# Kernel tuning notes

Measured on AMD Instinct MI355X. Metric: run time of the kernel, lower is better.

Reference implementation:

```python
import jax, jax.numpy as jnp
import numpy as np

N_NODES = 100000
N_EDGES = 1600000
D_IN = 128
D_OUT = 128


def setup_inputs() -> dict:
    key = jax.random.key(0)
    k1, k2, k3, k4, k5, k6 = jax.random.split(key, 6)
    x = jax.random.normal(k1, (N_NODES, D_IN), dtype=jnp.float32)
    edge_row = jax.random.randint(k2, (N_EDGES,), 0, N_NODES, dtype=jnp.int64)
    edge_col = jax.random.randint(k3, (N_EDGES,), 0, N_NODES, dtype=jnp.int64)
    edge_val = jax.random.uniform(k4, (N_EDGES,), dtype=jnp.float32)
    # Xavier-uniform init for weight, zeros for bias (matches reset_parameters)
    limit = float(np.sqrt(6.0 / (D_IN + D_OUT)))
    weight = jax.random.uniform(k5, (D_IN, D_OUT), minval=-limit, maxval=limit, dtype=jnp.float32)
    bias = jax.random.normal(k6, (D_OUT,), dtype=jnp.float32) * 0.02
    return {"x": x, "edge_row": edge_row, "edge_col": edge_col,
            "edge_val": edge_val, "weight": weight, "bias": bias}


def reference(x, edge_row, edge_col, edge_val, weight, bias):
    # dropout(p=0.0) is identity in eval -> omitted
    support = x @ weight                       # [N, D_OUT] dense GEMM
    # SpMM: out[r] = sum_{e: row[e]==r} val[e] * support[col[e]]
    messages = edge_val[:, None] * support[edge_col]   # [E, D_OUT]
    out = jax.ops.segment_sum(messages, edge_row, num_segments=N_NODES)
    return out + bias
```

## Files before the change

kernel.cpp:

```cpp
#include <hip/hip_runtime.h>


#define DMODEL 128
#define CAP 56
#define BROWS 256
#define BCAP 5120
#define NB_SC 800
#define SC_CHUNK 2000
#define SC_EPT 8
#define MAXBUCK 400

typedef __attribute__((ext_vector_type(8))) short short8_t;
typedef __attribute__((ext_vector_type(4))) float float4_t;

__device__ inline short f2bf(float f) {
    unsigned u = __float_as_uint(f);
    return (short)((u + 0x7FFFu + ((u >> 16) & 1u)) >> 16);
}

__global__ __launch_bounds__(256) void prep_kernel(const float* __restrict__ w,
                                                   unsigned short* __restrict__ wsw,
                                                   int* __restrict__ cursor, int nbuck) {
    if (blockIdx.x < 8) {
        int c = blockIdx.x * 256 + threadIdx.x;
        int lane = c & 63;
        int kcnt = c >> 6;
        int kc = kcnt & 3, nt = kcnt >> 2;
        int n  = nt * 16 + (lane & 15);
        int k0 = kc * 32 + (lane >> 4) * 8;
        short8_t v;
        #pragma unroll
        for (int j = 0; j < 8; ++j)
            v[j] = f2bf(w[(size_t)(k0 + j) * DMODEL + n]);
        *(short8_t*)&wsw[(size_t)c * 8] = v;
    } else {
        for (int j = threadIdx.x; j < nbuck; j += 256) cursor[j] = 0;
    }
}

__global__ __launch_bounds__(256) void scatter_kernel(
    const int* __restrict__ erow, const int* __restrict__ ecol,
    const float* __restrict__ eval,
    int* __restrict__ cursor, uint2* __restrict__ rec, int n_edges, int nbuck)
{
    __shared__ int cnt[MAXBUCK];
    __shared__ int gb[MAXBUCK];
    for (int j = threadIdx.x; j < nbuck; j += 256) cnt[j] = 0;
    __syncthreads();

    int base = blockIdx.x * SC_CHUNK;
    int lr[SC_EPT];
    #pragma unroll
    for (int i = 0; i < SC_EPT; ++i) {
        int e = base + threadIdx.x + i * 256;
        lr[i] = -1;
        if (threadIdx.x + i * 256 < SC_CHUNK && e < n_edges) {
            int b = erow[e] >> 8;
            lr[i] = atomicAdd(&cnt[b], 1);
        }
    }
    __syncthreads();
    for (int j = threadIdx.x; j < nbuck; j += 256) {
        int c = cnt[j];
        gb[j] = c ? atomicAdd(&cursor[j], c) : 0;
    }
    __syncthreads();
    #pragma unroll
    for (int i = 0; i < SC_EPT; ++i) {
        if (lr[i] >= 0) {
            int e = base + threadIdx.x + i * 256;
            int r = erow[e];
            int b = r >> 8;
            int pos = gb[b] + lr[i];
            if (pos < BCAP) {
                unsigned q = (unsigned)(eval[e] * 32767.0f + 0.5f);
                uint2 v;
                v.x = (q << 17) | (unsigned)ecol[e];
                v.y = (unsigned)(r & (BROWS - 1));
                rec[(size_t)b * BCAP + pos] = v;
            }
        }
    }
}

__global__ __launch_bounds__(256) void bucket_insert_kernel(
    const int* __restrict__ cursor, const uint2* __restrict__ rec,
    int* __restrict__ counts, unsigned* __restrict__ edata, int n_nodes)
{
    int b = blockIdx.x;
    __shared__ int cnt2[BROWS];
    cnt2[threadIdx.x] = 0;
    __syncthreads();

    int cb = cursor[b]; if (cb > BCAP) cb = BCAP;
    const uint2* rb = rec + (size_t)b * BCAP;
    for (int j = threadIdx.x; j < cb; j += 256) {
        uint2 v = rb[j];
        int rl = (int)v.y;
        int rk = atomicAdd(&cnt2[rl], 1);
        if (rk < CAP) {
            int row = (b << 8) + rl;
            edata[(size_t)row * CAP + rk] = v.x;
        }
    }
    __syncthreads();
    int row = (b << 8) + (int)threadIdx.x;
    if (row < n_nodes) counts[row] = cnt2[threadIdx.x];
}

__global__ __launch_bounds__(256) void gemm_kernel(
    const float* __restrict__ x, const unsigned short* __restrict__ wsw,
    unsigned short* __restrict__ support, int n_nodes)
{
    int wv   = threadIdx.x >> 6;
    int lane = threadIdx.x & 63;
    int m    = lane & 15;
    int g    = lane >> 4;

    int rowA  = blockIdx.x * 64 + wv * 16 + m;
    int rowAc = rowA < n_nodes ? rowA : n_nodes - 1;
    const float* xr = x + (size_t)rowAc * DMODEL + g * 8;

    short8_t af[4];
    #pragma unroll
    for (int kc = 0; kc < 4; ++kc) {
        float4 u0 = *(const float4*)(xr + kc * 32);
        float4 u1 = *(const float4*)(xr + kc * 32 + 4);
        short8_t a;
        a[0] = f2bf(u0.x); a[1] = f2bf(u0.y); a[2] = f2bf(u0.z); a[3] = f2bf(u0.w);
        a[4] = f2bf(u1.x); a[5] = f2bf(u1.y); a[6] = f2bf(u1.z); a[7] = f2bf(u1.w);
        af[kc] = a;
    }

    const short8_t* wf = (const short8_t*)wsw;

    float4_t acc[8];
    #pragma unroll
    for (int nt = 0; nt < 8; ++nt) {
        float4_t z = {0.f, 0.f, 0.f, 0.f};
        acc[nt] = z;
        #pragma unroll
        for (int kc = 0; kc < 4; ++kc) {
            short8_t bf = wf[(nt * 4 + kc) * 64 + lane];
            acc[nt] = __builtin_amdgcn_mfma_f32_16x16x32_bf16(af[kc], bf, acc[nt], 0, 0, 0);
        }
    }

    int orow = blockIdx.x * 64 + wv * 16 + g * 4;
    #pragma unroll
    for (int r = 0; r < 4; ++r) {
        int row = orow + r;
        if (row < n_nodes) {
            #pragma unroll
            for (int nt = 0; nt < 8; ++nt)
                support[(size_t)row * DMODEL + nt * 16 + m] = (unsigned short)f2bf(acc[nt][r]);
        }
    }
}

__global__ __launch_bounds__(256) void aggregate_kernel(
    const int* __restrict__ counts, const unsigned* __restrict__ edata,
    const uint4* __restrict__ sup, const float* __restrict__ bias,
    float* __restrict__ out, int n_nodes)
{
    int node = (blockIdx.x * blockDim.x + threadIdx.x) >> 6;
    if (node >= n_nodes) return;
    int lane = threadIdx.x & 63;
    int sub  = lane >> 4;
    int q    = lane & 15;

    int len = counts[node];
    if (len > CAP) len = CAP;
    const unsigned* ed = edata + (size_t)node * CAP;

    float acc[8];
    #pragma unroll
    for (int k = 0; k < 8; ++k) acc[k] = 0.f;

    const float SCL = 1.0f / 32767.0f;

    #define EDGE_FMA(rec, p)                                                 \
        {                                                                    \
            float v = (float)((rec) >> 17) * SCL;                            \
            acc[0] = fmaf(v, __uint_as_float((p).x << 16), acc[0]);          \
            acc[1] = fmaf(v, __uint_as_float((p).x & 0xFFFF0000u), acc[1]);  \
            acc[2] = fmaf(v, __uint_as_float((p).y << 16), acc[2]);          \
            acc[3] = fmaf(v, __uint_as_float((p).y & 0xFFFF0000u), acc[3]);  \
            acc[4] = fmaf(v, __uint_as_float((p).z << 16), acc[4]);          \
            acc[5] = fmaf(v, __uint_as_float((p).z & 0xFFFF0000u), acc[5]);  \
            acc[6] = fmaf(v, __uint_as_float((p).w << 16), acc[6]);          \
            acc[7] = fmaf(v, __uint_as_float((p).w & 0xFFFF0000u), acc[7]);  \
        }

    int i = sub;
    for (; i + 12 < len; i += 16) {
        unsigned r0 = ed[i];
        unsigned r1 = ed[i + 4];
        unsigned r2 = ed[i + 8];
        unsigned r3 = ed[i + 12];
        uint4 p0 = sup[(size_t)(r0 & 0x1FFFFu) * 16 + q];
        uint4 p1 = sup[(size_t)(r1 & 0x1FFFFu) * 16 + q];
        uint4 p2 = sup[(size_t)(r2 & 0x1FFFFu) * 16 + q];
        uint4 p3 = sup[(size_t)(r3 & 0x1FFFFu) * 16 + q];
        EDGE_FMA(r0, p0);
        EDGE_FMA(r1, p1);
        EDGE_FMA(r2, p2);
        EDGE_FMA(r3, p3);
    }
    for (; i < len; i += 4) {
        unsigned r0 = ed[i];
        uint4 p0 = sup[(size_t)(r0 & 0x1FFFFu) * 16 + q];
        EDGE_FMA(r0, p0);
    }
    #undef EDGE_FMA

    #pragma unroll
    for (int k = 0; k < 8; ++k) {
        acc[k] += __shfl_xor(acc[k], 16);
        acc[k] += __shfl_xor(acc[k], 32);
    }

    if (sub == 0) {
        float4 b0 = ((const float4*)bias)[q * 2];
        float4 b1 = ((const float4*)bias)[q * 2 + 1];
        float4_t o0 = {acc[0] + b0.x, acc[1] + b0.y, acc[2] + b0.z, acc[3] + b0.w};
        float4_t o1 = {acc[4] + b1.x, acc[5] + b1.y, acc[6] + b1.z, acc[7] + b1.w};
        __builtin_nontemporal_store(o0, (float4_t*)out + (size_t)node * 32 + q * 2);
        __builtin_nontemporal_store(o1, (float4_t*)out + (size_t)node * 32 + q * 2 + 1);
    }
}

extern "C" void kernel_launch(void* const* d_in, const int* in_sizes, int n_in,
                              void* d_out, int out_size, void* d_ws, size_t ws_size,
                              hipStream_t stream) {
    const float* x      = (const float*)d_in[0];
    const int*   erow   = (const int*)d_in[1];
    const int*   ecol   = (const int*)d_in[2];
    const float* eval   = (const float*)d_in[3];
    const float* weight = (const float*)d_in[4];
    const float* bias   = (const float*)d_in[5];
    float* out = (float*)d_out;

    const int n_nodes = in_sizes[0] / DMODEL;
    const int n_edges = in_sizes[3];
    const int nbuck   = (n_nodes + BROWS - 1) / BROWS;

    char* ws = (char*)d_ws;
    unsigned short* support = (unsigned short*)ws;
    uint2*          rec     = (uint2*)ws;
    ws += (size_t)n_nodes * DMODEL * 2;
    unsigned short* wsw     = (unsigned short*)ws;  ws += (size_t)DMODEL * DMODEL * 2;
    int*      counts = (int*)ws;                    ws += ((size_t)n_nodes * 4 + 15) & ~15ull;
    int*      cursor = (int*)ws;                    ws += ((size_t)nbuck * 4 + 15) & ~15ull;
    unsigned* edata  = (unsigned*)ws;               ws += (size_t)n_nodes * CAP * 4;

    const int nb_g = (n_nodes + 63) / 64;

    prep_kernel<<<9, 256, 0, stream>>>(weight, wsw, cursor, nbuck);
    scatter_kernel<<<NB_SC, 256, 0, stream>>>(erow, ecol, eval, cursor, rec, n_edges, nbuck);
    bucket_insert_kernel<<<nbuck, 256, 0, stream>>>(cursor, rec, counts, edata, n_nodes);
    gemm_kernel<<<nb_g, 256, 0, stream>>>(x, wsw, support, n_nodes);
    aggregate_kernel<<<(n_nodes + 3) / 4, 256, 0, stream>>>(
        counts, edata, (const uint4*)support, bias, out, n_nodes);
}
```

Measured before the change: 248.6 us.

## Slice support matrix by column blocks so aggregation gathers stay cache-resident

The GEMM now writes support in a column-sliced layout: 8 slices of 16 bf16 columns, each holding all nodes contiguously. Aggregation runs one block per (node chunk, slice), with 16 lanes per node, each lane pair covering a 32-byte row slice. Consecutive blocks cycle through slices, so each slice (about 3.2 MB) can stay hot in L2 during random gathers. The cost is that edge records are re-read once per slice, gathers shrink to 32-byte segments, and lane utilization drops for low-degree nodes.

```diff
diff --git a/kernel.cpp b/kernel.cpp
--- a/kernel.cpp
+++ b/kernel.cpp
@@ -9,6 +9,7 @@
 #define SC_CHUNK 2000
 #define SC_EPT 8
 #define MAXBUCK 400
+#define NSLICE 8
 
 typedef __attribute__((ext_vector_type(8))) short short8_t;
 typedef __attribute__((ext_vector_type(4))) float float4_t;
@@ -153,25 +154,29 @@
         if (row < n_nodes) {
             #pragma unroll
             for (int nt = 0; nt < 8; ++nt)
-                support[(size_t)row * DMODEL + nt * 16 + m] = (unsigned short)f2bf(acc[nt][r]);
+                support[((size_t)nt * n_nodes + row) * 16 + m] = (unsigned short)f2bf(acc[nt][r]);
         }
     }
 }
 
 __global__ __launch_bounds__(256) void aggregate_kernel(
     const int* __restrict__ counts, const unsigned* __restrict__ edata,
-    const uint4* __restrict__ sup, const float* __restrict__ bias,
+    const unsigned short* __restrict__ sup_s, const float* __restrict__ bias,
     float* __restrict__ out, int n_nodes)
 {
-    int node = (blockIdx.x * blockDim.x + threadIdx.x) >> 6;
+    int slice  = blockIdx.x & (NSLICE - 1);
+    int nchunk = blockIdx.x >> 3;
+    int grp  = threadIdx.x >> 4;
+    int node = nchunk * 16 + grp;
     if (node >= n_nodes) return;
-    int lane = threadIdx.x & 63;
-    int sub  = lane >> 4;
-    int q    = lane & 15;
+    int l    = threadIdx.x & 15;
+    int slot = l >> 1;
+    int half = l & 1;
 
     int len = counts[node];
     if (len > CAP) len = CAP;
     const unsigned* ed = edata + (size_t)node * CAP;
+    const unsigned short* sb = sup_s + (size_t)slice * n_nodes * 16;
 
     float acc[8];
     #pragma unroll
@@ -192,41 +197,38 @@
             acc[7] = fmaf(v, __uint_as_float((p).w & 0xFFFF0000u), acc[7]);  \
         }
 
-    int i = sub;
-    for (; i + 12 < len; i += 16) {
+    int i = slot;
+    for (; i + 8 < len; i += 16) {
         unsigned r0 = ed[i];
-        unsigned r1 = ed[i + 4];
-        unsigned r2 = ed[i + 8];
-        unsigned r3 = ed[i + 12];
-        uint4 p0 = sup[(size_t)(r0 & 0x1FFFFu) * 16 + q];
-        uint4 p1 = sup[(size_t)(r1 & 0x1FFFFu) * 16 + q];
-        uint4 p2 = sup[(size_t)(r2 & 0x1FFFFu) * 16 + q];
-        uint4 p3 = sup[(size_t)(r3 & 0x1FFFFu) * 16 + q];
+        unsigned r1 = ed[i + 8];
+        uint4 p0 = *(const uint4*)(sb + (size_t)(r0 & 0x1FFFFu) * 16 + half * 8);
+        uint4 p1 = *(const uint4*)(sb + (size_t)(r1 & 0x1FFFFu) * 16 + half * 8);
         EDGE_FMA(r0, p0);
         EDGE_FMA(r1, p1);
-        EDGE_FMA(r2, p2);
-        EDGE_FMA(r3, p3);
-    }
-    for (; i < len; i += 4) {
+    }
+    for (; i < len; i += 8) {
         unsigned r0 = ed[i];
-        uint4 p0 = sup[(size_t)(r0 & 0x1FFFFu) * 16 + q];
+        uint4 p0 = *(const uint4*)(sb + (size_t)(r0 & 0x1FFFFu) * 16 + half * 8);
         EDGE_FMA(r0, p0);
     }
     #undef EDGE_FMA
 
     #pragma unroll
     for (int k = 0; k < 8; ++k) {
-        acc[k] += __shfl_xor(acc[k], 16);
-        acc[k] += __shfl_xor(acc[k], 32);
-    }
-
-    if (sub == 0) {
-        float4 b0 = ((const float4*)bias)[q * 2];
-        float4 b1 = ((const float4*)bias)[q * 2 + 1];
+        acc[k] += __shfl_xor(acc[k], 2);
+        acc[k] += __shfl_xor(acc[k], 4);
+        acc[k] += __shfl_xor(acc[k], 8);
+    }
+
+    if (slot == 0) {
+        int col0 = slice * 16 + half * 8;
+        float4 b0 = *(const float4*)(bias + col0);
+        float4 b1 = *(const float4*)(bias + col0 + 4);
         float4_t o0 = {acc[0] + b0.x, acc[1] + b0.y, acc[2] + b0.z, acc[3] + b0.w};
         float4_t o1 = {acc[4] + b1.x, acc[5] + b1.y, acc[6] + b1.z, acc[7] + b1.w};
-        __builtin_nontemporal_store(o0, (float4_t*)out + (size_t)node * 32 + q * 2);
-        __builtin_nontemporal_store(o1, (float4_t*)out + (size_t)node * 32 + q * 2 + 1);
+        float* op = out + (size_t)node * DMODEL + col0;
+        __builtin_nontemporal_store(o0, (float4_t*)op);
+        __builtin_nontemporal_store(o1, (float4_t*)(op + 4));
     }
 }
 
@@ -254,12 +256,13 @@
     int*      cursor = (int*)ws;                    ws += ((size_t)nbuck * 4 + 15) & ~15ull;
     unsigned* edata  = (unsigned*)ws;               ws += (size_t)n_nodes * CAP * 4;
 
-    const int nb_g = (n_nodes + 63) / 64;
+    const int nb_g  = (n_nodes + 63) / 64;
+    const int nb_ag = NSLICE * ((n_nodes + 15) / 16);
 
     prep_kernel<<<9, 256, 0, stream>>>(weight, wsw, cursor, nbuck);
     scatter_kernel<<<NB_SC, 256, 0, stream>>>(erow, ecol, eval, cursor, rec, n_edges, nbuck);
     bucket_insert_kernel<<<nbuck, 256, 0, stream>>>(cursor, rec, counts, edata, n_nodes);
     gemm_kernel<<<nb_g, 256, 0, stream>>>(x, wsw, support, n_nodes);
-    aggregate_kernel<<<(n_nodes + 3) / 4, 256, 0, stream>>>(
-        counts, edata, (const uint4*)support, bias, out, n_nodes);
-}
+    aggregate_kernel<<<nb_ag, 256, 0, stream>>>(
+        counts, edata, support, bias, out, n_nodes);
+}
```

Result: slower. 289.8 us (+16.6%).

## Fuse bucket grouping into aggregation via shared-memory per-row edge lists

Applied to the files above, without the earlier changes.

Removes the bucket_insert kernel and the global edata/counts arrays. Each aggregation block now loads its bucket's records, groups them by row in LDS, and then aggregates 32 rows per wave. Buckets are halved to 128 rows, and each cursor counter is padded to its own cache line to cut atomic contention. This saves a kernel launch and a global write/read of the grouped edges. The cost is about 28KB of LDS per block, which limits occupancy, and fewer blocks (782) each doing serial per-node loops with long-latency gathers.

```diff
diff --git a/kernel.cpp b/kernel.cpp
--- a/kernel.cpp
+++ b/kernel.cpp
@@ -3,12 +3,14 @@
 
 #define DMODEL 128
 #define CAP 56
-#define BROWS 256
-#define BCAP 5120
+#define BROWS 128
+#define BSHIFT 7
+#define BCAP 2560
 #define NB_SC 800
 #define SC_CHUNK 2000
 #define SC_EPT 8
-#define MAXBUCK 400
+#define MAXBUCK 800
+#define CURPAD 16
 
 typedef __attribute__((ext_vector_type(8))) short short8_t;
 typedef __attribute__((ext_vector_type(4))) float float4_t;
@@ -20,7 +22,7 @@
 
 __global__ __launch_bounds__(256) void prep_kernel(const float* __restrict__ w,
                                                    unsigned short* __restrict__ wsw,
-                                                   int* __restrict__ cursor, int nbuck) {
+                                                   int* __restrict__ cursor, int n_cursor) {
     if (blockIdx.x < 8) {
         int c = blockIdx.x * 256 + threadIdx.x;
         int lane = c & 63;
@@ -34,7 +36,7 @@
             v[j] = f2bf(w[(size_t)(k0 + j) * DMODEL + n]);
         *(short8_t*)&wsw[(size_t)c * 8] = v;
     } else {
-        for (int j = threadIdx.x; j < nbuck; j += 256) cursor[j] = 0;
+        for (int j = threadIdx.x; j < n_cursor; j += 256) cursor[j] = 0;
     }
 }
 
@@ -55,14 +57,14 @@
         int e = base + threadIdx.x + i * 256;
         lr[i] = -1;
         if (threadIdx.x + i * 256 < SC_CHUNK && e < n_edges) {
-            int b = erow[e] >> 8;
+            int b = erow[e] >> BSHIFT;
             lr[i] = atomicAdd(&cnt[b], 1);
         }
     }
     __syncthreads();
     for (int j = threadIdx.x; j < nbuck; j += 256) {
         int c = cnt[j];
-        gb[j] = c ? atomicAdd(&cursor[j], c) : 0;
+        gb[j] = c ? atomicAdd(&cursor[j * CURPAD], c) : 0;
     }
     __syncthreads();
     #pragma unroll
@@ -70,7 +72,7 @@
         if (lr[i] >= 0) {
             int e = base + threadIdx.x + i * 256;
             int r = erow[e];
-            int b = r >> 8;
+            int b = r >> BSHIFT;
             int pos = gb[b] + lr[i];
             if (pos < BCAP) {
                 unsigned q = (unsigned)(eval[e] * 32767.0f + 0.5f);
@@ -83,31 +85,6 @@
     }
 }
 
-__global__ __launch_bounds__(256) void bucket_insert_kernel(
-    const int* __restrict__ cursor, const uint2* __restrict__ rec,
-    int* __restrict__ counts, unsigned* __restrict__ edata, int n_nodes)
-{
-    int b = blockIdx.x;
-    __shared__ int cnt2[BROWS];
-    cnt2[threadIdx.x] = 0;
-    __syncthreads();
-
-    int cb = cursor[b]; if (cb > BCAP) cb = BCAP;
-    const uint2* rb = rec + (size_t)b * BCAP;
-    for (int j = threadIdx.x; j < cb; j += 256) {
-        uint2 v = rb[j];
-        int rl = (int)v.y;
-        int rk = atomicAdd(&cnt2[rl], 1);
-        if (rk < CAP) {
-            int row = (b << 8) + rl;
-            edata[(size_t)row * CAP + rk] = v.x;
-        }
-    }
-    __syncthreads();
-    int row = (b << 8) + (int)threadIdx.x;
-    if (row < n_nodes) counts[row] = cnt2[threadIdx.x];
-}
-
 __global__ __launch_bounds__(256) void gemm_kernel(
     const float* __restrict__ x, const unsigned short* __restrict__ wsw,
     unsigned short* __restrict__ support, int n_nodes)
@@ -158,75 +135,94 @@
     }
 }
 
-__global__ __launch_bounds__(256) void aggregate_kernel(
-    const int* __restrict__ counts, const unsigned* __restrict__ edata,
+__global__ __launch_bounds__(256) void bucket_aggregate_kernel(
+    const int* __restrict__ cursor, const uint2* __restrict__ rec,
     const uint4* __restrict__ sup, const float* __restrict__ bias,
     float* __restrict__ out, int n_nodes)
 {
-    int node = (blockIdx.x * blockDim.x + threadIdx.x) >> 6;
-    if (node >= n_nodes) return;
+    int b = blockIdx.x;
+    __shared__ unsigned grouped[BROWS * CAP];
+    __shared__ int cnt[BROWS];
+    for (int j = threadIdx.x; j < BROWS; j += 256) cnt[j] = 0;
+    __syncthreads();
+
+    int cb = cursor[b * CURPAD]; if (cb > BCAP) cb = BCAP;
+    const uint2* rb = rec + (size_t)b * BCAP;
+    for (int j = threadIdx.x; j < cb; j += 256) {
+        uint2 v = rb[j];
+        int rl = (int)v.y;
+        int rk = atomicAdd(&cnt[rl], 1);
+        if (rk < CAP) grouped[rl * CAP + rk] = v.x;
+    }
+    __syncthreads();
+
+    int wv   = threadIdx.x >> 6;
     int lane = threadIdx.x & 63;
     int sub  = lane >> 4;
     int q    = lane & 15;
 
-    int len = counts[node];
-    if (len > CAP) len = CAP;
-    const unsigned* ed = edata + (size_t)node * CAP;
-
-    float acc[8];
-    #pragma unroll
-    for (int k = 0; k < 8; ++k) acc[k] = 0.f;
-
     const float SCL = 1.0f / 32767.0f;
 
-    #define EDGE_FMA(rec, p)                                                 \
-        {                                                                    \
-            float v = (float)((rec) >> 17) * SCL;                            \
-            acc[0] = fmaf(v, __uint_as_float((p).x << 16), acc[0]);          \
-            acc[1] = fmaf(v, __uint_as_float((p).x & 0xFFFF0000u), acc[1]);  \
-            acc[2] = fmaf(v, __uint_as_float((p).y << 16), acc[2]);          \
-            acc[3] = fmaf(v, __uint_as_float((p).y & 0xFFFF0000u), acc[3]);  \
-            acc[4] = fmaf(v, __uint_as_float((p).z << 16), acc[4]);          \
-            acc[5] = fmaf(v, __uint_as_float((p).z & 0xFFFF0000u), acc[5]);  \
-            acc[6] = fmaf(v, __uint_as_float((p).w << 16), acc[6]);          \
-            acc[7] = fmaf(v, __uint_as_float((p).w & 0xFFFF0000u), acc[7]);  \
-        }
-
-    int i = sub;
-    for (; i + 12 < len; i += 16) {
-        unsigned r0 = ed[i];
-        unsigned r1 = ed[i + 4];
-        unsigned r2 = ed[i + 8];
-        unsigned r3 = ed[i + 12];
-        uint4 p0 = sup[(size_t)(r0 & 0x1FFFFu) * 16 + q];
-        uint4 p1 = sup[(size_t)(r1 & 0x1FFFFu) * 16 + q];
-        uint4 p2 = sup[(size_t)(r2 & 0x1FFFFu) * 16 + q];
-        uint4 p3 = sup[(size_t)(r3 & 0x1FFFFu) * 16 + q];
-        EDGE_FMA(r0, p0);
-        EDGE_FMA(r1, p1);
-        EDGE_FMA(r2, p2);
-        EDGE_FMA(r3, p3);
-    }
-    for (; i < len; i += 4) {
-        unsigned r0 = ed[i];
-        uint4 p0 = sup[(size_t)(r0 & 0x1FFFFu) * 16 + q];
-        EDGE_FMA(r0, p0);
-    }
-    #undef EDGE_FMA
-
-    #pragma unroll
-    for (int k = 0; k < 8; ++k) {
-        acc[k] += __shfl_xor(acc[k], 16);
-        acc[k] += __shfl_xor(acc[k], 32);
-    }
-
-    if (sub == 0) {
-        float4 b0 = ((const float4*)bias)[q * 2];
-        float4 b1 = ((const float4*)bias)[q * 2 + 1];
-        float4_t o0 = {acc[0] + b0.x, acc[1] + b0.y, acc[2] + b0.z, acc[3] + b0.w};
-        float4_t o1 = {acc[4] + b1.x, acc[5] + b1.y, acc[6] + b1.z, acc[7] + b1.w};
-        __builtin_nontemporal_store(o0, (float4_t*)out + (size_t)node * 32 + q * 2);
-        __builtin_nontemporal_store(o1, (float4_t*)out + (size_t)node * 32 + q * 2 + 1);
+    for (int nl = wv * 32; nl < wv * 32 + 32; ++nl) {
+        int node = (b << BSHIFT) + nl;
+        if (node >= n_nodes) break;
+        int len = cnt[nl];
+        if (len > CAP) len = CAP;
+        const unsigned* ed = &grouped[nl * CAP];
+
+        float acc[8];
+        #pragma unroll
+        for (int k = 0; k < 8; ++k) acc[k] = 0.f;
+
+        #define EDGE_FMA(rec_, p)                                                \
+            {                                                                    \
+                float v = (float)((rec_) >> 17) * SCL;                           \
+                acc[0] = fmaf(v, __uint_as_float((p).x << 16), acc[0]);          \
+                acc[1] = fmaf(v, __uint_as_float((p).x & 0xFFFF0000u), acc[1]);  \
+                acc[2] = fmaf(v, __uint_as_float((p).y << 16), acc[2]);          \
+                acc[3] = fmaf(v, __uint_as_float((p).y & 0xFFFF0000u), acc[3]);  \
+                acc[4] = fmaf(v, __uint_as_float((p).z << 16), acc[4]);          \
+                acc[5] = fmaf(v, __uint_as_float((p).z & 0xFFFF0000u), acc[5]);  \
+                acc[6] = fmaf(v, __uint_as_float((p).w << 16), acc[6]);          \
+                acc[7] = fmaf(v, __uint_as_float((p).w & 0xFFFF0000u), acc[7]);  \
+            }
+
+        int i = sub;
+        for (; i + 12 < len; i += 16) {
+            unsigned r0 = ed[i];
+            unsigned r1 = ed[i + 4];
+            unsigned r2 = ed[i + 8];
+            unsigned r3 = ed[i + 12];
+            uint4 p0 = sup[(size_t)(r0 & 0x1FFFFu) * 16 + q];
+            uint4 p1 = sup[(size_t)(r1 & 0x1FFFFu) * 16 + q];
+            uint4 p2 = sup[(size_t)(r2 & 0x1FFFFu) * 16 + q];
+            uint4 p3 = sup[(size_t)(r3 & 0x1FFFFu) * 16 + q];
+            EDGE_FMA(r0, p0);
+            EDGE_FMA(r1, p1);
+            EDGE_FMA(r2, p2);
+            EDGE_FMA(r3, p3);
+        }
+        for (; i < len; i += 4) {
+            unsigned r0 = ed[i];
+            uint4 p0 = sup[(size_t)(r0 & 0x1FFFFu) * 16 + q];
+            EDGE_FMA(r0, p0);
+        }
+        #undef EDGE_FMA
+
+        #pragma unroll
+        for (int k = 0; k < 8; ++k) {
+            acc[k] += __shfl_xor(acc[k], 16);
+            acc[k] += __shfl_xor(acc[k], 32);
+        }
+
+        if (sub == 0) {
+            float4 b0 = ((const float4*)bias)[q * 2];
+            float4 b1 = ((const float4*)bias)[q * 2 + 1];
+            float4_t o0 = {acc[0] + b0.x, acc[1] + b0.y, acc[2] + b0.z, acc[3] + b0.w};
+            float4_t o1 = {acc[4] + b1.x, acc[5] + b1.y, acc[6] + b1.z, acc[7] + b1.w};
+            __builtin_nontemporal_store(o0, (float4_t*)out + (size_t)node * 32 + q * 2);
+            __builtin_nontemporal_store(o1, (float4_t*)out + (size_t)node * 32 + q * 2 + 1);
+        }
     }
 }
 
@@ -246,20 +242,17 @@
     const int nbuck   = (n_nodes + BROWS - 1) / BROWS;
 
     char* ws = (char*)d_ws;
-    unsigned short* support = (unsigned short*)ws;
-    uint2*          rec     = (uint2*)ws;
-    ws += (size_t)n_nodes * DMODEL * 2;
+    unsigned short* support = (unsigned short*)ws;  ws += (size_t)n_nodes * DMODEL * 2;
     unsigned short* wsw     = (unsigned short*)ws;  ws += (size_t)DMODEL * DMODEL * 2;
-    int*      counts = (int*)ws;                    ws += ((size_t)n_nodes * 4 + 15) & ~15ull;
-    int*      cursor = (int*)ws;                    ws += ((size_t)nbuck * 4 + 15) & ~15ull;
-    unsigned* edata  = (unsigned*)ws;               ws += (size_t)n_nodes * CAP * 4;
+    int*      cursor = (int*)ws;                    ws += ((size_t)nbuck * CURPAD * 4 + 63) & ~63ull;
+    uint2*    rec    = (uint2*)ws;                  ws += (size_t)nbuck * BCAP * 8;
 
     const int nb_g = (n_nodes + 63) / 64;
-
-    prep_kernel<<<9, 256, 0, stream>>>(weight, wsw, cursor, nbuck);
+    const int n_cursor = nbuck * CURPAD;
+
+    prep_kernel<<<9, 256, 0, stream>>>(weight, wsw, cursor, n_cursor);
     scatter_kernel<<<NB_SC, 256, 0, stream>>>(erow, ecol, eval, cursor, rec, n_edges, nbuck);
-    bucket_insert_kernel<<<nbuck, 256, 0, stream>>>(cursor, rec, counts, edata, n_nodes);
     gemm_kernel<<<nb_g, 256, 0, stream>>>(x, wsw, support, n_nodes);
-    aggregate_kernel<<<(n_nodes + 3) / 4, 256, 0, stream>>>(
-        counts, edata, (const uint4*)support, bias, out, n_nodes);
-}
+    bucket_aggregate_kernel<<<nbuck, 256, 0, stream>>>(
+        cursor, rec, (const uint4*)support, bias, out, n_nodes);
+}
```

After: 265.7 us. +6.9%, slower.
